# Kernel tuning notes

Measured on AMD Instinct MI355X. Metric: run time of the kernel, lower is better.

## Reference

```python
import jax, jax.numpy as jnp
import numpy as np


def _he_scale(k, shape, fan_in):
    return jax.random.normal(k, shape, dtype=jnp.float32) * np.sqrt(2.0 / fan_in).astype(np.float32)


def setup_inputs() -> dict:
    key = jax.random.key(0)
    kx, kt, kp, kg, kf = jax.random.split(key, 5)
    B, H, W, C, D = 4, 64, 64, 256, 128
    x = jax.random.normal(kx, (B, H, W, C), dtype=jnp.float32)
    Wt = _he_scale(kt, (C, D), C)
    Wp = _he_scale(kp, (C, D), C)
    Wg = _he_scale(kg, (C, D), C)
    Wf = _he_scale(kf, (D, C), D)
    return {"x": x, "Wt": Wt, "Wp": Wp, "Wg": Wg, "Wf": Wf}


def _maxpool1d(z, pool_size=2, stride=1):
    # Keras MaxPool1D, padding='valid': output length = (N - pool_size)//stride + 1
    return jax.lax.reduce_window(
        z, -jnp.inf, jax.lax.max,
        window_dimensions=(1, pool_size, 1),
        window_strides=(1, stride, 1),
        padding='VALID')


def reference(x, Wt, Wp, Wg, Wf):
    B, H, W, C = x.shape
    D = Wt.shape[1]
    N = H * W
    # 1x1 conv projections == per-position matmuls
    theta = jnp.einsum('bhwc,cd->bhwd', x, Wt).reshape(B, N, D)   # [B,N,D]
    phi = jnp.einsum('bhwc,cd->bhwd', x, Wp).reshape(B, N, D)     # [B,N,D]
    g = jnp.einsum('bhwc,cd->bhwd', x, Wg).reshape(B, N, D)       # [B,N,D]
    # embedded mode: subsample phi and g (pool_size=2, strides=1) -> M = N-1
    phi = _maxpool1d(phi)                                          # [B,M,D]
    g = _maxpool1d(g)                                              # [B,M,D]
    # f = theta @ phi^T, softmax over keys (no scaling in embedded mode)
    f = jax.nn.softmax(jnp.einsum('bnd,bmd->bnm', theta, phi), axis=-1)  # [B,N,M]
    y = jnp.einsum('bnm,bmd->bnd', f, g).reshape(B, H, W, D)       # [B,H,W,D]
    # final 1x1 conv back to C channels + residual
    z = x + jnp.einsum('bhwd,dc->bhwc', y, Wf)
    return z
```

## Files before the change

### kernel.cpp

```cpp
#include <hip/hip_runtime.h>

#define B_  4
#define N_  4096
#define C_  256
#define D_  128
#define M_  4095
#define BN_ (B_ * N_)
#define KSPLIT 4

typedef _Float16 half_t;
typedef __attribute__((ext_vector_type(8))) _Float16 half8;
typedef __attribute__((ext_vector_type(4))) _Float16 half4;
typedef __attribute__((ext_vector_type(4))) float f32x4;

#define MFMA16x16x32(A, B, C) __builtin_amdgcn_mfma_f32_16x16x32_f16(A, B, C, 0, 0, 0)
#define LOG2E 1.44269504088896f

__global__ __launch_bounds__(256) void prep_kernel(
    const float* __restrict__ Wt, const float* __restrict__ Wp,
    const float* __restrict__ Wg, const float* __restrict__ Wf,
    half_t* __restrict__ WT_hi, half_t* __restrict__ WfT)
{
    const int idx = blockIdx.x * 256 + threadIdx.x;
    const int wsel = blockIdx.y;
    if (wsel < 3) {
        const float* __restrict__ W = (wsel == 0) ? Wt : (wsel == 1) ? Wp : Wg;
        const int d = idx >> 8, c = idx & 255;
        WT_hi[(size_t)wsel * 32768 + idx] = (half_t)W[(size_t)c * D_ + d];
    } else {
        const int c = idx >> 7, d = idx & 127;
        WfT[idx] = (half_t)Wf[(size_t)d * C_ + c];
    }
}

__global__ __launch_bounds__(256) void proj_kernel(
    const float* __restrict__ x, const half_t* __restrict__ WT_hi,
    half_t* __restrict__ theta, half_t* __restrict__ pphi,
    half_t* __restrict__ pgT)
{
    const int tid = threadIdx.x;
    const int lane = tid & 63;
    const int w = tid >> 6;
    const int lm = lane & 15;
    const int lq = lane >> 4;
    const int r0 = blockIdx.x * 64;
    const int which = blockIdx.y;
    const half_t* __restrict__ Wg_ = WT_hi + (size_t)which * 32768;

    __shared__ __align__(16) unsigned char lds_raw[18432];
    half_t (*Xh)[40]  = (half_t (*)[40])(lds_raw);
    half_t (*Whl)[40] = (half_t (*)[40])(lds_raw + 5120);

    f32x4 acc[8];
#pragma unroll
    for (int nb = 0; nb < 8; ++nb)
#pragma unroll
        for (int r = 0; r < 4; ++r) acc[nb][r] = 0.f;

    const int xr = tid >> 2, xc = (tid & 3) * 8;
    const int wr = tid >> 1, wc = (tid & 1) * 16;

    for (int kc = 0; kc < 8; ++kc) {
        __syncthreads();
        {
            const float* xs = x + (size_t)(r0 + xr) * C_ + kc * 32 + xc;
            float4 v0 = *(const float4*)&xs[0], v1 = *(const float4*)&xs[4];
            half8 hi;
            hi[0] = (half_t)v0.x; hi[1] = (half_t)v0.y;
            hi[2] = (half_t)v0.z; hi[3] = (half_t)v0.w;
            hi[4] = (half_t)v1.x; hi[5] = (half_t)v1.y;
            hi[6] = (half_t)v1.z; hi[7] = (half_t)v1.w;
            *(half8*)&Xh[xr][xc] = hi;
            const half_t* wsrc = Wg_ + (size_t)wr * 256 + kc * 32 + wc;
            *(half8*)&Whl[wr][wc]     = *(const half8*)&wsrc[0];
            *(half8*)&Whl[wr][wc + 8] = *(const half8*)&wsrc[8];
        }
        __syncthreads();

        half8 ah = *(const half8*)&Xh[w * 16 + lm][lq * 8];
#pragma unroll
        for (int nb = 0; nb < 8; ++nb) {
            half8 bh = *(const half8*)&Whl[nb * 16 + lm][lq * 8];
            acc[nb] = MFMA16x16x32(ah, bh, acc[nb]);
        }
    }

    if (which == 0) {
#pragma unroll
        for (int nb = 0; nb < 8; ++nb)
#pragma unroll
            for (int r = 0; r < 4; ++r)
                theta[(size_t)(r0 + w * 16 + lq * 4 + r) * D_ + nb * 16 + lm] =
                    (half_t)(acc[nb][r] * LOG2E);
        return;
    }

    __syncthreads();
    half_t (*LsT)[72] = (half_t (*)[72])(lds_raw);
#pragma unroll
    for (int nb = 0; nb < 8; ++nb) {
        const int d = nb * 16 + lm;
        const int m = w * 16 + lq * 4;
        half4 pk;
#pragma unroll
        for (int r = 0; r < 4; ++r) pk[r] = (half_t)acc[nb][r];
        *(half4*)&LsT[d][m] = pk;
    }
    if (tid < 128) {
        int rh = r0 + 64;
        if ((rh & (N_ - 1)) == 0) rh = r0 + 63;
        const float* xrow = x + (size_t)rh * C_;
        const half_t* wrow = Wg_ + (size_t)tid * 256;
        float s = 0.f;
#pragma unroll
        for (int c8 = 0; c8 < 32; ++c8) {
            half8 h = *(const half8*)&wrow[c8 * 8];
            float4 xa = *(const float4*)&xrow[c8 * 8];
            float4 xb = *(const float4*)&xrow[c8 * 8 + 4];
            s += xa.x * (float)h[0] + xa.y * (float)h[1]
               + xa.z * (float)h[2] + xa.w * (float)h[3]
               + xb.x * (float)h[4] + xb.y * (float)h[5]
               + xb.z * (float)h[6] + xb.w * (float)h[7];
        }
        LsT[tid][64] = (half_t)s;
    }
    __syncthreads();

    if (which == 1) {
        const int m = tid >> 2, dh = (tid & 3) * 32;
        half8 o[4];
#pragma unroll
        for (int j = 0; j < 32; ++j) {
            float v0 = (float)LsT[dh + j][m];
            float v1 = (float)LsT[dh + j][m + 1];
            o[j >> 3][j & 7] = (half_t)fmaxf(v0, v1);
        }
        half8* dst = (half8*)&pphi[(size_t)(r0 + m) * D_ + dh];
#pragma unroll
        for (int j = 0; j < 4; ++j) dst[j] = o[j];
    } else {
        const int d = tid >> 1, mh = (tid & 1) * 32;
        const int b = r0 / N_, m0 = r0 & (N_ - 1);
        half8 in[4];
#pragma unroll
        for (int j = 0; j < 4; ++j) in[j] = *(const half8*)&LsT[d][mh + j * 8];
        const half_t ext = LsT[d][mh + 32];
        half8 o[4];
#pragma unroll
        for (int j = 0; j < 32; ++j) {
            float v0 = (float)in[j >> 3][j & 7];
            float v1 = (j == 31) ? (float)ext : (float)in[(j + 1) >> 3][(j + 1) & 7];
            o[j >> 3][j & 7] = (half_t)fmaxf(v0, v1);
        }
        half8* dst = (half8*)&pgT[((size_t)b * D_ + d) * N_ + m0 + mh];
#pragma unroll
        for (int j = 0; j < 4; ++j) dst[j] = o[j];
    }
}

__global__ __launch_bounds__(256, 2) void attn_kernel(
    const half_t* __restrict__ theta, const half_t* __restrict__ pphi,
    const half_t* __restrict__ pgT, half_t* __restrict__ ypart,
    float* __restrict__ mstat, float* __restrict__ lstat)
{
    const int tid = threadIdx.x;
    const int lane = tid & 63;
    const int w = tid >> 6;
    const int lm = lane & 15;
    const int lq = lane >> 4;
    const int qt = blockIdx.x, ksb = blockIdx.y, b = blockIdx.z;
    const int q0 = qt * 128;
    const int kt0 = ksb * 16, kt1 = kt0 + 16;

    __shared__ half_t Ks[64][136];
    __shared__ half_t Gts[128][72];
    __shared__ half_t Ps[128][72];

    half8 qh[2][4];
#pragma unroll
    for (int nb = 0; nb < 2; ++nb) {
        const half_t* tr_ = theta + ((size_t)b * N_ + q0 + w * 32 + nb * 16 + lm) * D_;
#pragma unroll
        for (int k4 = 0; k4 < 4; ++k4)
            qh[nb][k4] = *(const half8*)(tr_ + k4 * 32 + lq * 8);
    }

    float m_i[2] = {-1e30f, -1e30f};
    float l_i[2] = {0.f, 0.f};
    f32x4 yacc[2][8];
#pragma unroll
    for (int mb = 0; mb < 2; ++mb)
#pragma unroll
        for (int dn = 0; dn < 8; ++dn)
#pragma unroll
            for (int r = 0; r < 4; ++r) yacc[mb][dn][r] = 0.f;

    for (int kt = kt0; kt < kt1; ++kt) {
        const int k0 = kt * 64;
        __syncthreads();
        {
            const int key = tid >> 2, ch = (tid & 3);
            const float4* src = (const float4*)(pphi +
                ((size_t)b * N_ + k0 + key) * D_ + ch * 32);
            float4 a0 = src[0], a1 = src[1], a2 = src[2], a3 = src[3];
            float4* dst = (float4*)&Ks[key][ch * 32];
            dst[0] = a0; dst[1] = a1; dst[2] = a2; dst[3] = a3;
            const int d = tid >> 1, kh = (tid & 1);
            const float4* gs = (const float4*)(pgT +
                ((size_t)b * D_ + d) * N_ + k0 + kh * 32);
            float4 g0 = gs[0], g1 = gs[1], g2 = gs[2], g3 = gs[3];
            float4* gd = (float4*)&Gts[d][kh * 32];
            gd[0] = g0; gd[1] = g1; gd[2] = g2; gd[3] = g3;
        }
        __syncthreads();

        f32x4 sc[4][2];
#pragma unroll
        for (int kb = 0; kb < 4; ++kb)
#pragma unroll
            for (int nb = 0; nb < 2; ++nb)
#pragma unroll
                for (int r = 0; r < 4; ++r) sc[kb][nb][r] = 0.f;
#pragma unroll
        for (int kb = 0; kb < 4; ++kb) {
#pragma unroll
            for (int k4 = 0; k4 < 4; ++k4) {
                half8 kf = *(const half8*)&Ks[kb * 16 + lm][k4 * 32 + lq * 8];
#pragma unroll
                for (int nb = 0; nb < 2; ++nb)
                    sc[kb][nb] = MFMA16x16x32(kf, qh[nb][k4], sc[kb][nb]);
            }
        }
        if (k0 + 64 > M_) {
#pragma unroll
            for (int kb = 0; kb < 4; ++kb)
#pragma unroll
                for (int r = 0; r < 4; ++r)
                    if (k0 + kb * 16 + lq * 4 + r >= M_) {
                        sc[kb][0][r] = -1e30f; sc[kb][1][r] = -1e30f;
                    }
        }
        float alpha[2];
#pragma unroll
        for (int nb = 0; nb < 2; ++nb) {
            float mt = -1e30f;
#pragma unroll
            for (int kb = 0; kb < 4; ++kb)
#pragma unroll
                for (int r = 0; r < 4; ++r) mt = fmaxf(mt, sc[kb][nb][r]);
            mt = fmaxf(mt, __shfl_xor(mt, 16, 64));
            mt = fmaxf(mt, __shfl_xor(mt, 32, 64));
            const float mnew = fmaxf(m_i[nb], mt);
            alpha[nb] = exp2f(m_i[nb] - mnew);
            m_i[nb] = mnew;
            float rs = 0.f;
#pragma unroll
            for (int kb = 0; kb < 4; ++kb)
#pragma unroll
                for (int r = 0; r < 4; ++r) {
                    float p = exp2f(sc[kb][nb][r] - mnew);
                    sc[kb][nb][r] = p;
                    rs += p;
                }
            l_i[nb] = l_i[nb] * alpha[nb] + rs;
#pragma unroll
            for (int kb = 0; kb < 4; ++kb) {
                half4 pk;
#pragma unroll
                for (int r = 0; r < 4; ++r) pk[r] = (half_t)sc[kb][nb][r];
                *(half4*)&Ps[w * 32 + nb * 16 + lm][kb * 16 + lq * 4] = pk;
            }
        }
        float alpha_t[2][4];
#pragma unroll
        for (int mb = 0; mb < 2; ++mb)
#pragma unroll
            for (int r = 0; r < 4; ++r)
                alpha_t[mb][r] = __shfl(alpha[mb], lq * 4 + r, 16);
#pragma unroll
        for (int mb = 0; mb < 2; ++mb)
#pragma unroll
            for (int dn = 0; dn < 8; ++dn)
#pragma unroll
                for (int r = 0; r < 4; ++r) yacc[mb][dn][r] *= alpha_t[mb][r];
        half8 pf[2][2];
#pragma unroll
        for (int mb = 0; mb < 2; ++mb)
#pragma unroll
            for (int k2 = 0; k2 < 2; ++k2)
                pf[mb][k2] = *(const half8*)&Ps[w * 32 + mb * 16 + lm][k2 * 32 + lq * 8];
#pragma unroll
        for (int dn = 0; dn < 8; ++dn) {
#pragma unroll
            for (int k2 = 0; k2 < 2; ++k2) {
                half8 gf = *(const half8*)&Gts[dn * 16 + lm][k2 * 32 + lq * 8];
                yacc[0][dn] = MFMA16x16x32(pf[0][k2], gf, yacc[0][dn]);
                yacc[1][dn] = MFMA16x16x32(pf[1][k2], gf, yacc[1][dn]);
            }
        }
    }

#pragma unroll
    for (int nb = 0; nb < 2; ++nb) {
        l_i[nb] += __shfl_xor(l_i[nb], 16, 64);
        l_i[nb] += __shfl_xor(l_i[nb], 32, 64);
    }
    half_t* yp = ypart + ((size_t)ksb * BN_ + (size_t)b * N_) * D_;
#pragma unroll
    for (int mb = 0; mb < 2; ++mb)
#pragma unroll
        for (int dn = 0; dn < 8; ++dn)
#pragma unroll
            for (int r = 0; r < 4; ++r)
                yp[(size_t)(q0 + w * 32 + mb * 16 + lq * 4 + r) * D_ + dn * 16 + lm] =
                    (half_t)yacc[mb][dn][r];
    if (lq == 0) {
#pragma unroll
        for (int nb = 0; nb < 2; ++nb) {
            const int row = q0 + w * 32 + nb * 16 + lm;
            mstat[(size_t)ksb * BN_ + (size_t)b * N_ + row] = m_i[nb];
            lstat[(size_t)ksb * BN_ + (size_t)b * N_ + row] = l_i[nb];
        }
    }
}

__global__ __launch_bounds__(256) void final_kernel(
    const half_t* __restrict__ ypart, const float* __restrict__ mstat,
    const float* __restrict__ lstat, const float* __restrict__ x,
    const half_t* __restrict__ WfT, float* __restrict__ out)
{
    const int tid = threadIdx.x;
    const int lane = tid & 63;
    const int w = tid >> 6;
    const int lm = lane & 15;
    const int lq = lane >> 4;
    const int r0 = blockIdx.x * 128;
    const int c0 = blockIdx.y * 128;

    __shared__ half_t Ys[128][72];
    __shared__ half_t Wfs[128][72];
    __shared__ float scl[KSPLIT][128];

    if (tid < 128) {
        const int row = r0 + tid;
        float mv[KSPLIT], lv[KSPLIT], wv[KSPLIT];
        float Mx = -1e30f;
#pragma unroll
        for (int s = 0; s < KSPLIT; ++s) {
            mv[s] = mstat[(size_t)s * BN_ + row];
            lv[s] = lstat[(size_t)s * BN_ + row];
            Mx = fmaxf(Mx, mv[s]);
        }
        float lsum = 0.f;
#pragma unroll
        for (int s = 0; s < KSPLIT; ++s) { wv[s] = exp2f(mv[s] - Mx); lsum += wv[s] * lv[s]; }
        const float inv = 1.f / lsum;
#pragma unroll
        for (int s = 0; s < KSPLIT; ++s) scl[s][tid] = wv[s] * inv;
    }
    __syncthreads();

    f32x4 acc[2][8];
#pragma unroll
    for (int rb = 0; rb < 2; ++rb)
#pragma unroll
        for (int nb = 0; nb < 8; ++nb)
#pragma unroll
            for (int r = 0; r < 4; ++r) acc[rb][nb][r] = 0.f;

    const int sr = tid >> 1;
    const int dd = (tid & 1) * 32;

    for (int kc = 0; kc < 2; ++kc) {
        {
            float ss[KSPLIT];
#pragma unroll
            for (int s = 0; s < KSPLIT; ++s) ss[s] = scl[s][sr];
            const size_t yb = (size_t)(r0 + sr) * D_ + kc * 64 + dd;
            half8 o[4];
#pragma unroll
            for (int q = 0; q < 4; ++q) {
                float m[8];
#pragma unroll
                for (int j = 0; j < 8; ++j) m[j] = 0.f;
#pragma unroll
                for (int s = 0; s < KSPLIT; ++s) {
                    half8 yv = *(const half8*)&ypart[(size_t)s * BN_ * D_ + yb + q * 8];
#pragma unroll
                    for (int j = 0; j < 8; ++j) m[j] += ss[s] * (float)yv[j];
                }
#pragma unroll
                for (int j = 0; j < 8; ++j) o[q][j] = (half_t)m[j];
            }
#pragma unroll
            for (int q = 0; q < 4; ++q) *(half8*)&Ys[sr][dd + q * 8] = o[q];
            const half_t* wf = WfT + (size_t)(c0 + sr) * D_ + kc * 64 + dd;
#pragma unroll
            for (int q = 0; q < 4; ++q)
                *(half8*)&Wfs[sr][dd + q * 8] = *(const half8*)&wf[q * 8];
        }
        __syncthreads();

        half8 af[2][2];
#pragma unroll
        for (int rb = 0; rb < 2; ++rb)
#pragma unroll
            for (int k2 = 0; k2 < 2; ++k2)
                af[rb][k2] = *(const half8*)&Ys[w * 32 + rb * 16 + lm][k2 * 32 + lq * 8];
#pragma unroll
        for (int nb = 0; nb < 8; ++nb) {
#pragma unroll
            for (int k2 = 0; k2 < 2; ++k2) {
                half8 bf = *(const half8*)&Wfs[nb * 16 + lm][k2 * 32 + lq * 8];
                acc[0][nb] = MFMA16x16x32(af[0][k2], bf, acc[0][nb]);
                acc[1][nb] = MFMA16x16x32(af[1][k2], bf, acc[1][nb]);
            }
        }
        __syncthreads();
    }
#pragma unroll
    for (int rb = 0; rb < 2; ++rb)
#pragma unroll
        for (int nb = 0; nb < 8; ++nb)
#pragma unroll
            for (int r = 0; r < 4; ++r) {
                const int row = r0 + w * 32 + rb * 16 + lq * 4 + r;
                const int col = c0 + nb * 16 + lm;
                out[(size_t)row * C_ + col] =
                    acc[rb][nb][r] + x[(size_t)row * C_ + col];
            }
}

extern "C" void kernel_launch(void* const* d_in, const int* in_sizes, int n_in,
                              void* d_out, int out_size, void* d_ws, size_t ws_size,
                              hipStream_t stream)
{
    const float* x  = (const float*)d_in[0];
    const float* Wt = (const float*)d_in[1];
    const float* Wp = (const float*)d_in[2];
    const float* Wg = (const float*)d_in[3];
    const float* Wf = (const float*)d_in[4];
    float* out = (float*)d_out;

    const size_t SEG = (size_t)BN_ * D_;
    float* ws     = (float*)d_ws;
    half_t* theta = (half_t*)ws;
    half_t* pphi  = (half_t*)(ws + SEG / 2);
    half_t* pgT   = (half_t*)(ws + SEG);
    half_t* ypart = (half_t*)(ws + SEG + SEG / 2);
    float* mstat  = ws + 3 * SEG + SEG / 2;
    float* lstat  = mstat + (size_t)KSPLIT * BN_;
    half_t* WT_hi = (half_t*)(lstat + (size_t)KSPLIT * BN_);
    half_t* WfT   = WT_hi + 3 * 32768;

    prep_kernel<<<dim3(128, 4), 256, 0, stream>>>(Wt, Wp, Wg, Wf, WT_hi, WfT);
    proj_kernel<<<dim3(BN_ / 64, 3), 256, 0, stream>>>(x, WT_hi, theta, pphi, pgT);
    attn_kernel<<<dim3(N_ / 128, KSPLIT, B_), 256, 0, stream>>>(
        theta, pphi, pgT, ypart, mstat, lstat);
    final_kernel<<<dim3(BN_ / 128, 2), 256, 0, stream>>>(
        ypart, mstat, lstat, x, WfT, out);
}
```

Baseline: 177.1 us.

## Register-prefetch next tiles in projection and attention loops; lazy softmax rescale

In the projection GEMM and the flash-attention loop, the next tile of global data is now loaded into registers while the current tile is computed, then written to LDS after the compute. This hides global load latency behind the MFMA work. The attention loop also skips updating the running max and rescaling the accumulators unless some row's tile max exceeds the stored max by a threshold (FA4-style lazy rescale). That removes exp2 and multiply work but lets unnormalized values grow up to 2^5, which adds some fp16 overflow and precision risk.

```diff
diff --git a/kernel.cpp b/kernel.cpp
--- a/kernel.cpp
+++ b/kernel.cpp
@@ -15,6 +15,7 @@
 
 #define MFMA16x16x32(A, B, C) __builtin_amdgcn_mfma_f32_16x16x32_f16(A, B, C, 0, 0, 0)
 #define LOG2E 1.44269504088896f
+#define RTHR  5.0f
 
 __global__ __launch_bounds__(256) void prep_kernel(
     const float* __restrict__ Wt, const float* __restrict__ Wp,
@@ -60,20 +61,30 @@
     const int xr = tid >> 2, xc = (tid & 3) * 8;
     const int wr = tid >> 1, wc = (tid & 1) * 16;
 
+    const float* xs = x + (size_t)(r0 + xr) * C_ + xc;
+    const half_t* wsrc = Wg_ + (size_t)wr * 256 + wc;
+    float4 xv0 = *(const float4*)&xs[0];
+    float4 xv1 = *(const float4*)&xs[4];
+    half8 wv0 = *(const half8*)&wsrc[0];
+    half8 wv1 = *(const half8*)&wsrc[8];
+
     for (int kc = 0; kc < 8; ++kc) {
+        half8 hi;
+        hi[0] = (half_t)xv0.x; hi[1] = (half_t)xv0.y;
+        hi[2] = (half_t)xv0.z; hi[3] = (half_t)xv0.w;
+        hi[4] = (half_t)xv1.x; hi[5] = (half_t)xv1.y;
+        hi[6] = (half_t)xv1.z; hi[7] = (half_t)xv1.w;
+        half8 w0 = wv0, w1 = wv1;
         __syncthreads();
-        {
-            const float* xs = x + (size_t)(r0 + xr) * C_ + kc * 32 + xc;
-            float4 v0 = *(const float4*)&xs[0], v1 = *(const float4*)&xs[4];
-            half8 hi;
-            hi[0] = (half_t)v0.x; hi[1] = (half_t)v0.y;
-            hi[2] = (half_t)v0.z; hi[3] = (half_t)v0.w;
-            hi[4] = (half_t)v1.x; hi[5] = (half_t)v1.y;
-            hi[6] = (half_t)v1.z; hi[7] = (half_t)v1.w;
-            *(half8*)&Xh[xr][xc] = hi;
-            const half_t* wsrc = Wg_ + (size_t)wr * 256 + kc * 32 + wc;
-            *(half8*)&Whl[wr][wc]     = *(const half8*)&wsrc[0];
-            *(half8*)&Whl[wr][wc + 8] = *(const half8*)&wsrc[8];
+        *(half8*)&Xh[xr][xc] = hi;
+        *(half8*)&Whl[wr][wc]     = w0;
+        *(half8*)&Whl[wr][wc + 8] = w1;
+        if (kc < 7) {
+            xs += 32; wsrc += 32;
+            xv0 = *(const float4*)&xs[0];
+            xv1 = *(const float4*)&xs[4];
+            wv0 = *(const half8*)&wsrc[0];
+            wv1 = *(const half8*)&wsrc[8];
         }
         __syncthreads();
 
@@ -185,6 +196,26 @@
             qh[nb][k4] = *(const half8*)(tr_ + k4 * 32 + lq * 8);
     }
 
+    const int key = tid >> 2, ch = tid & 3;
+    const int gdd = tid >> 1, gkh = tid & 1;
+    const float4* ksrc = (const float4*)(pphi +
+        ((size_t)b * N_ + kt0 * 64 + key) * D_ + ch * 32);
+    const float4* gsrc = (const float4*)(pgT +
+        ((size_t)b * D_ + gdd) * N_ + kt0 * 64 + gkh * 32);
+
+    float4 kr[4], gr[4];
+#pragma unroll
+    for (int j = 0; j < 4; ++j) { kr[j] = ksrc[j]; gr[j] = gsrc[j]; }
+    ksrc += 1024;
+    gsrc += 8;
+    {
+        float4* kdst = (float4*)&Ks[key][ch * 32];
+        float4* gdst = (float4*)&Gts[gdd][gkh * 32];
+#pragma unroll
+        for (int j = 0; j < 4; ++j) { kdst[j] = kr[j]; gdst[j] = gr[j]; }
+    }
+    __syncthreads();
+
     float m_i[2] = {-1e30f, -1e30f};
     float l_i[2] = {0.f, 0.f};
     f32x4 yacc[2][8];
@@ -197,22 +228,13 @@
 
     for (int kt = kt0; kt < kt1; ++kt) {
         const int k0 = kt * 64;
-        __syncthreads();
-        {
-            const int key = tid >> 2, ch = (tid & 3);
-            const float4* src = (const float4*)(pphi +
-                ((size_t)b * N_ + k0 + key) * D_ + ch * 32);
-            float4 a0 = src[0], a1 = src[1], a2 = src[2], a3 = src[3];
-            float4* dst = (float4*)&Ks[key][ch * 32];
-            dst[0] = a0; dst[1] = a1; dst[2] = a2; dst[3] = a3;
-            const int d = tid >> 1, kh = (tid & 1);
-            const float4* gs = (const float4*)(pgT +
-                ((size_t)b * D_ + d) * N_ + k0 + kh * 32);
-            float4 g0 = gs[0], g1 = gs[1], g2 = gs[2], g3 = gs[3];
-            float4* gd = (float4*)&Gts[d][kh * 32];
-            gd[0] = g0; gd[1] = g1; gd[2] = g2; gd[3] = g3;
-        }
-        __syncthreads();
+        const bool has_next = (kt + 1 < kt1);
+
+        if (has_next) {
+#pragma unroll
+            for (int j = 0; j < 4; ++j) { kr[j] = ksrc[j]; gr[j] = gsrc[j]; }
+            ksrc += 1024; gsrc += 8;
+        }
 
         f32x4 sc[4][2];
 #pragma unroll
@@ -240,49 +262,64 @@
                         sc[kb][0][r] = -1e30f; sc[kb][1][r] = -1e30f;
                     }
         }
-        float alpha[2];
+
+        float mt[2];
 #pragma unroll
         for (int nb = 0; nb < 2; ++nb) {
-            float mt = -1e30f;
+            float m0 = -1e30f;
 #pragma unroll
             for (int kb = 0; kb < 4; ++kb)
 #pragma unroll
-                for (int r = 0; r < 4; ++r) mt = fmaxf(mt, sc[kb][nb][r]);
-            mt = fmaxf(mt, __shfl_xor(mt, 16, 64));
-            mt = fmaxf(mt, __shfl_xor(mt, 32, 64));
-            const float mnew = fmaxf(m_i[nb], mt);
-            alpha[nb] = exp2f(m_i[nb] - mnew);
-            m_i[nb] = mnew;
+                for (int r = 0; r < 4; ++r) m0 = fmaxf(m0, sc[kb][nb][r]);
+            m0 = fmaxf(m0, __shfl_xor(m0, 16, 64));
+            m0 = fmaxf(m0, __shfl_xor(m0, 32, 64));
+            mt[nb] = m0;
+        }
+        const bool need0 = __any(mt[0] > m_i[0] + RTHR);
+        const bool need1 = __any(mt[1] > m_i[1] + RTHR);
+        float alphav[2] = {1.f, 1.f};
+#pragma unroll
+        for (int nb = 0; nb < 2; ++nb) {
+            const bool need = nb ? need1 : need0;
+            float mnew = m_i[nb];
+            if (need) {
+                mnew = fmaxf(m_i[nb], mt[nb]);
+                alphav[nb] = exp2f(m_i[nb] - mnew);
+                m_i[nb] = mnew;
+            }
             float rs = 0.f;
 #pragma unroll
-            for (int kb = 0; kb < 4; ++kb)
+            for (int kb = 0; kb < 4; ++kb) {
+                half4 pk;
 #pragma unroll
                 for (int r = 0; r < 4; ++r) {
                     float p = exp2f(sc[kb][nb][r] - mnew);
-                    sc[kb][nb][r] = p;
                     rs += p;
+                    pk[r] = (half_t)p;
                 }
-            l_i[nb] = l_i[nb] * alpha[nb] + rs;
-#pragma unroll
-            for (int kb = 0; kb < 4; ++kb) {
-                half4 pk;
-#pragma unroll
-                for (int r = 0; r < 4; ++r) pk[r] = (half_t)sc[kb][nb][r];
                 *(half4*)&Ps[w * 32 + nb * 16 + lm][kb * 16 + lq * 4] = pk;
             }
-        }
-        float alpha_t[2][4];
-#pragma unroll
-        for (int mb = 0; mb < 2; ++mb)
-#pragma unroll
-            for (int r = 0; r < 4; ++r)
-                alpha_t[mb][r] = __shfl(alpha[mb], lq * 4 + r, 16);
-#pragma unroll
-        for (int mb = 0; mb < 2; ++mb)
+            l_i[nb] = l_i[nb] * alphav[nb] + rs;
+        }
+        if (need0) {
+            float a_t[4];
+#pragma unroll
+            for (int r = 0; r < 4; ++r) a_t[r] = __shfl(alphav[0], lq * 4 + r, 16);
 #pragma unroll
             for (int dn = 0; dn < 8; ++dn)
 #pragma unroll
-                for (int r = 0; r < 4; ++r) yacc[mb][dn][r] *= alpha_t[mb][r];
+                for (int r = 0; r < 4; ++r) yacc[0][dn][r] *= a_t[r];
+        }
+        if (need1) {
+            float a_t[4];
+#pragma unroll
+            for (int r = 0; r < 4; ++r) a_t[r] = __shfl(alphav[1], lq * 4 + r, 16);
+#pragma unroll
+            for (int dn = 0; dn < 8; ++dn)
+#pragma unroll
+                for (int r = 0; r < 4; ++r) yacc[1][dn][r] *= a_t[r];
+        }
+
         half8 pf[2][2];
 #pragma unroll
         for (int mb = 0; mb < 2; ++mb)
@@ -297,6 +334,15 @@
                 yacc[0][dn] = MFMA16x16x32(pf[0][k2], gf, yacc[0][dn]);
                 yacc[1][dn] = MFMA16x16x32(pf[1][k2], gf, yacc[1][dn]);
             }
+        }
+
+        if (has_next) {
+            __syncthreads();
+            float4* kdst = (float4*)&Ks[key][ch * 32];
+            float4* gdst = (float4*)&Gts[gdd][gkh * 32];
+#pragma unroll
+            for (int j = 0; j < 4; ++j) { kdst[j] = kr[j]; gdst[j] = gr[j]; }
+            __syncthreads();
         }
     }
 
```

After: 209.5 us. 1.18x slower.
